# Kernel tuning notes

Measured on AMD Instinct MI355X. Metric: run time of the kernel, lower is better.

The kernel has to match this reference:

```python
import jax, jax.numpy as jnp
import numpy as np

# layer hyperparameters (init_kwargs)
SCORE_T = 0.05
IOU_T = 0.5
MAX_OUT = 300
BBOX_STD = np.array([0.1, 0.1, 0.2, 0.2], dtype=np.float32)


def setup_inputs() -> dict:
    key = jax.random.key(0)
    k1, k2, k3, k4 = jax.random.split(key, 4)
    B, N, C = 8, 2000, 81
    deltas = jax.random.normal(k1, (B, N, C, 4), jnp.float32) * 0.1
    class_logits = jax.random.normal(k2, (B, N, C), jnp.float32)
    # well-formed proposal boxes (y1,x1,y2,x2) in normalized coords + tag column
    cyx = jax.random.uniform(k3, (B, N, 2), jnp.float32, 0.1, 0.9)
    hw = jax.random.uniform(k4, (B, N, 2), jnp.float32, 0.05, 0.3)
    proposals = jnp.concatenate([cyx - hw * 0.5, cyx + hw * 0.5, jnp.ones((B, N, 1), jnp.float32)], axis=-1)
    return {"deltas": deltas, "class_logits": class_logits, "proposals": proposals}


def apply_regress(d, boxes):
    # d: [...,4] (dy,dx,dh,dw); boxes: [...,4] (y1,x1,y2,x2)
    h = boxes[..., 2] - boxes[..., 0]
    w = boxes[..., 3] - boxes[..., 1]
    cy = (boxes[..., 2] + boxes[..., 0]) * 0.5
    cx = (boxes[..., 3] + boxes[..., 1]) * 0.5
    d = d * jnp.asarray(BBOX_STD, d.dtype)
    cy = cy + d[..., 0] * h
    cx = cx + d[..., 1] * w
    h = h * jnp.exp(d[..., 2])
    w = w * jnp.exp(d[..., 3])
    return jnp.stack([cy - h * 0.5, cx - w * 0.5, cy + h * 0.5, cx + w * 0.5], axis=-1)


def box_iou(a, b):
    # a: [N,4], b: [M,4] -> [N,M]
    yx1 = jnp.maximum(a[:, None, :2], b[None, :, :2])
    yx2 = jnp.minimum(a[:, None, 2:], b[None, :, 2:])
    inter = jnp.prod(jnp.maximum(yx2 - yx1, 0.0), axis=-1)
    area_a = (a[:, 2] - a[:, 0]) * (a[:, 3] - a[:, 1])
    area_b = (b[:, 2] - b[:, 0]) * (b[:, 3] - b[:, 1])
    return inter / (area_a[:, None] + area_b[None, :] - inter + 1e-8)


def nms_one(boxes, scores, logits):
    # boxes [N,4], scores [N], logits [N,C]; greedy NMS, pad to MAX_OUT with tag column
    ious = box_iou(boxes, boxes)  # [N,N]
    live = jnp.where(scores > SCORE_T, scores, -1.0)

    def step(s, _):
        idx = jnp.argmax(s)
        ok = s[idx] > 0.0  # softmax scores are >0; -1.0 marks dead
        s = jnp.where(ious[idx] > IOU_T, -1.0, s)
        s = s.at[idx].set(-1.0)
        return s, (idx, ok)

    _, (idxs, oks) = jax.lax.scan(step, live, None, length=MAX_OUT)
    okf = oks.astype(boxes.dtype)[:, None]  # [MAX_OUT,1], 1=real box, 0=padding
    out_boxes = jnp.concatenate([boxes[idxs] * okf, okf], axis=-1)          # [MAX_OUT,5]
    out_scores = jnp.concatenate([scores[idxs][:, None] * okf, okf], axis=-1)  # [MAX_OUT,2]
    out_logits = logits[idxs] * okf                                          # [MAX_OUT,C]
    return out_boxes, out_scores, out_logits


def reference(deltas, class_logits, proposals):
    boxes_in = proposals[..., :-1]                         # drop tag -> [B,N,4]
    class_scores = jax.nn.softmax(class_logits, axis=-1)   # [B,N,C]
    fg_scores = jnp.max(class_scores[..., 1:], axis=-1)    # [B,N]
    fg_cls = jnp.argmax(class_scores[..., 1:], axis=-1) + 1  # [B,N] best fg class
    # select class-specific delta for the best foreground class
    sel_deltas = jnp.take_along_axis(deltas, fg_cls[..., None, None], axis=2)[..., 0, :]  # [B,N,4]
    detect_boxes = apply_regress(sel_deltas, boxes_in)      # [B,N,4]
    return jax.vmap(nms_one)(detect_boxes, fg_scores, class_logits)
```

## Files before the change

### kernel.cpp

```cpp
#include <hip/hip_runtime.h>

#define BATCH 8
#define NBOX 2000
#define NCLS 81
#define NPAD 2048
#define MAX_OUT 300
#define SCORE_T 0.05f
#define IOU_T 0.5f
#define MASK_WORDS 64

#define WS_BOXES   0
#define WS_SCORES  256000
#define WS_SKEY    320000
#define WS_SBOX    451072
#define WS_LARR    713216
#define WS_KLIST   713248
#define WS_KCOUNT  722848
#define WS_MASK    786432

__global__ void prep_kernel(const float* __restrict__ deltas,
                            const float* __restrict__ logits,
                            const float* __restrict__ proposals,
                            float4* __restrict__ boxes_out,
                            float* __restrict__ scores_out,
                            int* __restrict__ Larr) {
    int bn = blockIdx.x * blockDim.x + threadIdx.x;
    if (bn < BATCH) Larr[bn] = 0;
    if (bn >= BATCH * NBOX) return;

    const float* l = logits + (long)bn * NCLS;

    float M = l[0];
    #pragma unroll 4
    for (int c = 1; c < NCLS; ++c) M = fmaxf(M, l[c]);

    float S = 0.0f;
    float bl = -3.0e38f; int bc = 1;
    #pragma unroll 4
    for (int c = 0; c < NCLS; ++c) {
        float v = l[c];
        S += expf(v - M);
        if (c >= 1 && v > bl) { bl = v; bc = c; }
    }
    float score = expf(bl - M) / S;

    const float* p = proposals + (long)bn * 5;
    float y1 = p[0], x1 = p[1], y2 = p[2], x2 = p[3];
    float h = y2 - y1, w = x2 - x1;
    float cy = (y2 + y1) * 0.5f, cx = (x2 + x1) * 0.5f;

    const float* d = deltas + ((long)bn * NCLS + bc) * 4;
    float d0 = d[0] * 0.1f, d1 = d[1] * 0.1f, d2 = d[2] * 0.2f, d3 = d[3] * 0.2f;

    cy = cy + d0 * h;
    cx = cx + d1 * w;
    h = h * expf(d2);
    w = w * expf(d3);

    boxes_out[bn] = make_float4(cy - h * 0.5f, cx - w * 0.5f,
                                cy + h * 0.5f, cx + w * 0.5f);
    scores_out[bn] = score;
}

__global__ __launch_bounds__(512) void rank_kernel(
        const float* __restrict__ scores,
        const float4* __restrict__ boxes,
        unsigned long long* __restrict__ skey,
        float4* __restrict__ sbox,
        int* __restrict__ Larr) {
    int bid = blockIdx.x;
    int b = bid & 7, rb = bid >> 3;
    int t = threadIdx.x;

    __shared__ unsigned long long s_key[NPAD + 16];
    __shared__ int s_part[64][8];

    for (int c = t; c < NPAD; c += 512) {
        unsigned int bits = 0u;
        if (c < NBOX) bits = __float_as_uint(scores[b * NBOX + c]);
        s_key[c + (c >> 7)] =
            ((unsigned long long)bits << 32) |
            (unsigned long long)(0xFFFFFFFFu - (unsigned)c);
    }
    __syncthreads();

    int own = rb * 64 + (t >> 3);
    int seg = t & 7;
    unsigned long long mykey = s_key[own + (own >> 7)];
    int cnt = 0;
    int cbase = seg * 256;
    #pragma unroll 4
    for (int j = 0; j < 256; ++j) {
        int c = cbase + j;
        cnt += (s_key[c + (c >> 7)] > mykey) ? 1 : 0;
    }
    s_part[t >> 3][seg] = cnt;
    __syncthreads();

    if (t < 64) {
        int own2 = rb * 64 + t;
        unsigned long long key = s_key[own2 + (own2 >> 7)];
        int rank = s_part[t][0] + s_part[t][1] + s_part[t][2] + s_part[t][3]
                 + s_part[t][4] + s_part[t][5] + s_part[t][6] + s_part[t][7];
        skey[b * NPAD + rank] = key;
        unsigned int orig = 0xFFFFFFFFu - (unsigned int)key;
        float4 bx = make_float4(0.f, 0.f, 0.f, 0.f);
        if (orig < NBOX) bx = boxes[b * NBOX + orig];
        sbox[b * NPAD + rank] = bx;
        float sc = __uint_as_float((unsigned int)(key >> 32));
        if (sc > SCORE_T) atomicMax(&Larr[b], rank + 1);
    }
}

__global__ __launch_bounds__(512) void mask_kernel(
        const float4* __restrict__ sbox,
        const int* __restrict__ Larr,
        unsigned int* __restrict__ mask) {
    int bid = blockIdx.x;
    int b = bid & 7, rb = bid >> 3;
    int L = Larr[b];
    if (rb * 64 >= L) return;
    int t = threadIdx.x;

    __shared__ float4 s_bx[NPAD + 16];

    for (int c = t; c < NPAD; c += 512)
        s_bx[c + (c >> 7)] = sbox[b * NPAD + c];
    __syncthreads();

    int r   = rb * 64 + (t & 63);
    int seg = t >> 6;
    float4 rbx = s_bx[r + (r >> 7)];
    float rar = (rbx.z - rbx.x) * (rbx.w - rbx.y);
    unsigned int* outp = mask + (((size_t)(b * NPAD + r)) << 6);

    for (int w = 0; w < 8; ++w) {
        int wi = (seg << 3) + w;
        unsigned int bits = 0u;
        int colbase = wi << 5;
        if (colbase + 31 > r && colbase < L) {
            #pragma unroll 8
            for (int c2 = 0; c2 < 32; ++c2) {
                int col = colbase + c2;
                float4 ob = s_bx[col + (col >> 7)];
                float oa = (ob.z - ob.x) * (ob.w - ob.y);
                float yy1 = fmaxf(rbx.x, ob.x), xx1 = fmaxf(rbx.y, ob.y);
                float yy2 = fminf(rbx.z, ob.z), xx2 = fminf(rbx.w, ob.w);
                float inter = fmaxf(yy2 - yy1, 0.f) * fmaxf(xx2 - xx1, 0.f);
                float iou = inter / (rar + oa - inter + 1e-8f);
                bits |= (iou > IOU_T) ? (1u << c2) : 0u;
            }
        }
        outp[wi] = bits;
    }
}

__global__ __launch_bounds__(64) void walk_kernel(
        const int* __restrict__ Larr,
        const unsigned int* __restrict__ mask,
        int* __restrict__ klist,
        int* __restrict__ kcount) {
    int b = blockIdx.x;
    int lane = threadIdx.x;

    int L = Larr[b];
    int nset = L - (lane << 5);
    nset = nset < 0 ? 0 : (nset > 32 ? 32 : nset);
    unsigned int alive = (nset >= 32) ? 0xFFFFFFFFu
                        : ((nset <= 0) ? 0u : ((1u << nset) - 1u));

    const unsigned int* M = mask + ((size_t)b * NPAD) * MASK_WORDS;
    int* kl = klist + b * MAX_OUT;
    int kept = 0;

#define EXTRACT(cd)                                                          \
    {                                                                        \
        if (!aw && ne) {                                                     \
            int _w = (int)__builtin_ctzll(ne); ne &= ne - 1ull;              \
            wbase = _w << 5;                                                 \
            aw = (unsigned int)__builtin_amdgcn_readlane((int)alive, _w);    \
        }                                                                    \
        if (aw) { cd = wbase + (int)__builtin_ctz(aw); aw &= aw - 1u; }      \
    }
#define COMMIT(cd, rowd)                                                     \
    if (cd >= 0 && kept < MAX_OUT) {                                         \
        unsigned int _av =                                                   \
            (unsigned int)__builtin_amdgcn_readlane((int)alive, cd >> 5);    \
        if (_av & (1u << (cd & 31))) {                                       \
            if (lane == 0) kl[kept] = cd;                                    \
            kept++;                                                          \
            alive &= ~rowd;                                                  \
            if (lane == (cd >> 5)) alive &= ~(1u << (cd & 31));              \
        }                                                                    \
    }

    while (kept < MAX_OUT) {
        unsigned long long ne = __ballot(alive != 0u);
        if (!ne) break;
        unsigned int aw = 0u;
        int wbase = 0;
        int c0 = -1, c1 = -1, c2 = -1, c3 = -1, c4 = -1, c5 = -1,
            c6 = -1, c7 = -1, c8 = -1, c9 = -1, c10 = -1, c11 = -1;
        EXTRACT(c0); EXTRACT(c1); EXTRACT(c2); EXTRACT(c3);
        EXTRACT(c4); EXTRACT(c5); EXTRACT(c6); EXTRACT(c7);
        EXTRACT(c8); EXTRACT(c9); EXTRACT(c10); EXTRACT(c11);

        int s1 = (c1 >= 0) ? c1 : c0;
        int s2 = (c2 >= 0) ? c2 : c0;
        int s3 = (c3 >= 0) ? c3 : c0;
        int s4 = (c4 >= 0) ? c4 : c0;
        int s5 = (c5 >= 0) ? c5 : c0;
        int s6 = (c6 >= 0) ? c6 : c0;
        int s7 = (c7 >= 0) ? c7 : c0;
        int s8 = (c8 >= 0) ? c8 : c0;
        int s9 = (c9 >= 0) ? c9 : c0;
        int s10 = (c10 >= 0) ? c10 : c0;
        int s11 = (c11 >= 0) ? c11 : c0;

        unsigned int row0  = M[((size_t)c0  << 6) + lane];
        unsigned int row1  = M[((size_t)s1  << 6) + lane];
        unsigned int row2  = M[((size_t)s2  << 6) + lane];
        unsigned int row3  = M[((size_t)s3  << 6) + lane];
        unsigned int row4  = M[((size_t)s4  << 6) + lane];
        unsigned int row5  = M[((size_t)s5  << 6) + lane];
        unsigned int row6  = M[((size_t)s6  << 6) + lane];
        unsigned int row7  = M[((size_t)s7  << 6) + lane];
        unsigned int row8  = M[((size_t)s8  << 6) + lane];
        unsigned int row9  = M[((size_t)s9  << 6) + lane];
        unsigned int row10 = M[((size_t)s10 << 6) + lane];
        unsigned int row11 = M[((size_t)s11 << 6) + lane];

        if (lane == 0) kl[kept] = c0;
        kept++;
        alive &= ~row0;
        if (lane == (c0 >> 5)) alive &= ~(1u << (c0 & 31));

        COMMIT(c1, row1);  COMMIT(c2, row2);  COMMIT(c3, row3);
        COMMIT(c4, row4);  COMMIT(c5, row5);  COMMIT(c6, row6);
        COMMIT(c7, row7);  COMMIT(c8, row8);  COMMIT(c9, row9);
        COMMIT(c10, row10); COMMIT(c11, row11);
    }
#undef EXTRACT
#undef COMMIT

    if (lane == 0) kcount[b] = kept;
}

__global__ void out_kernel(const unsigned long long* __restrict__ skey,
                           const float4* __restrict__ sbox,
                           const int* __restrict__ klist,
                           const int* __restrict__ kcount,
                           const float* __restrict__ logits,
                           float* __restrict__ out) {
    int idx = blockIdx.x * blockDim.x + threadIdx.x;
    const int NB = BATCH * MAX_OUT * 5;
    const int NS = BATCH * MAX_OUT * 2;
    const int NL = BATCH * MAX_OUT * NCLS;
    if (idx >= NB + NS + NL) return;

    if (idx < NB) {
        int b = idx / (MAX_OUT * 5);
        int rem = idx - b * (MAX_OUT * 5);
        int k = rem / 5, c = rem - 5 * k;
        float v = 0.f;
        if (k < kcount[b]) {
            if (c == 4) v = 1.f;
            else {
                float4 bx = sbox[b * NPAD + klist[b * MAX_OUT + k]];
                v = (c == 0) ? bx.x : (c == 1) ? bx.y : (c == 2) ? bx.z : bx.w;
            }
        }
        out[idx] = v;
    } else if (idx < NB + NS) {
        int j = idx - NB;
        int b = j / (MAX_OUT * 2);
        int rem = j - b * (MAX_OUT * 2);
        int k = rem >> 1, c = rem & 1;
        float v = 0.f;
        if (k < kcount[b]) {
            if (c) v = 1.f;
            else {
                unsigned long long key = skey[b * NPAD + klist[b * MAX_OUT + k]];
                v = __uint_as_float((unsigned int)(key >> 32));
            }
        }
        out[idx] = v;
    } else {
        int j = idx - NB - NS;
        int b = j / (MAX_OUT * NCLS);
        int rem = j - b * (MAX_OUT * NCLS);
        int k = rem / NCLS, c = rem - NCLS * k;
        float v = 0.f;
        if (k < kcount[b]) {
            unsigned long long key = skey[b * NPAD + klist[b * MAX_OUT + k]];
            unsigned int orig = 0xFFFFFFFFu - (unsigned int)key;
            v = logits[((long)b * NBOX + orig) * NCLS + c];
        }
        out[idx] = v;
    }
}

extern "C" void kernel_launch(void* const* d_in, const int* in_sizes, int n_in,
                              void* d_out, int out_size, void* d_ws, size_t ws_size,
                              hipStream_t stream) {
    const float* deltas    = (const float*)d_in[0];
    const float* logits    = (const float*)d_in[1];
    const float* proposals = (const float*)d_in[2];
    float* out = (float*)d_out;

    char* ws = (char*)d_ws;
    float4* ws_boxes  = (float4*)(ws + WS_BOXES);
    float*  ws_scores = (float*)(ws + WS_SCORES);
    unsigned long long* ws_skey = (unsigned long long*)(ws + WS_SKEY);
    float4* ws_sbox   = (float4*)(ws + WS_SBOX);
    int*    ws_Larr   = (int*)(ws + WS_LARR);
    int*    ws_klist  = (int*)(ws + WS_KLIST);
    int*    ws_kcount = (int*)(ws + WS_KCOUNT);
    unsigned int* ws_mask = (unsigned int*)(ws + WS_MASK);

    prep_kernel<<<(BATCH * NBOX + 255) / 256, 256, 0, stream>>>(
        deltas, logits, proposals, ws_boxes, ws_scores, ws_Larr);
    rank_kernel<<<BATCH * (NPAD / 64), 512, 0, stream>>>(
        ws_scores, ws_boxes, ws_skey, ws_sbox, ws_Larr);
    mask_kernel<<<BATCH * (NPAD / 64), 512, 0, stream>>>(
        ws_sbox, ws_Larr, ws_mask);
    walk_kernel<<<BATCH, 64, 0, stream>>>(
        ws_Larr, ws_mask, ws_klist, ws_kcount);
    int total_out = BATCH * MAX_OUT * (5 + 2 + NCLS);
    out_kernel<<<(total_out + 255) / 256, 256, 0, stream>>>(
        ws_skey, ws_sbox, ws_klist, ws_kcount, logits, out);
}
```

Measured before the change: 117.1 us.

## Resolve NMS walk in 64-candidate windows using ballot-built suppression submatrix

Restructures the greedy NMS walk kernel. Each iteration gathers up to 64 alive candidates through a prefix scan into shared memory and loads their mask rows plus the transposed column bits. It builds a 64x64 suppression submatrix with ballots, so the greedy keep/suppress decisions inside the window resolve in registers. This replaces the old loop that speculated on 12 candidates per iteration, cutting the number of serial iterations and dependent global loads per kept box. The cost is 128 global loads per lane per iteration, heavy register use (arrays of 64), several syncthreads, and wasted work when few candidates survive.

```diff
diff --git a/kernel.cpp b/kernel.cpp
--- a/kernel.cpp
+++ b/kernel.cpp
@@ -8,6 +8,7 @@
 #define SCORE_T 0.05f
 #define IOU_T 0.5f
 #define MASK_WORDS 64
+#define WDEPTH 64
 
 #define WS_BOXES   0
 #define WS_SCORES  256000
@@ -163,6 +164,10 @@
     int b = blockIdx.x;
     int lane = threadIdx.x;
 
+    __shared__ int s_cand[WDEPTH];
+    __shared__ unsigned int s_clrw[64];
+    __shared__ int s_kl[MAX_OUT];
+
     int L = Larr[b];
     int nset = L - (lane << 5);
     nset = nset < 0 ? 0 : (nset > 32 ? 32 : nset);
@@ -170,80 +175,110 @@
                         : ((nset <= 0) ? 0u : ((1u << nset) - 1u));
 
     const unsigned int* M = mask + ((size_t)b * NPAD) * MASK_WORDS;
-    int* kl = klist + b * MAX_OUT;
     int kept = 0;
-
-#define EXTRACT(cd)                                                          \
-    {                                                                        \
-        if (!aw && ne) {                                                     \
-            int _w = (int)__builtin_ctzll(ne); ne &= ne - 1ull;              \
-            wbase = _w << 5;                                                 \
-            aw = (unsigned int)__builtin_amdgcn_readlane((int)alive, _w);    \
-        }                                                                    \
-        if (aw) { cd = wbase + (int)__builtin_ctz(aw); aw &= aw - 1u; }      \
-    }
-#define COMMIT(cd, rowd)                                                     \
-    if (cd >= 0 && kept < MAX_OUT) {                                         \
-        unsigned int _av =                                                   \
-            (unsigned int)__builtin_amdgcn_readlane((int)alive, cd >> 5);    \
-        if (_av & (1u << (cd & 31))) {                                       \
-            if (lane == 0) kl[kept] = cd;                                    \
-            kept++;                                                          \
-            alive &= ~rowd;                                                  \
-            if (lane == (cd >> 5)) alive &= ~(1u << (cd & 31));              \
-        }                                                                    \
-    }
 
     while (kept < MAX_OUT) {
         unsigned long long ne = __ballot(alive != 0u);
         if (!ne) break;
-        unsigned int aw = 0u;
-        int wbase = 0;
-        int c0 = -1, c1 = -1, c2 = -1, c3 = -1, c4 = -1, c5 = -1,
-            c6 = -1, c7 = -1, c8 = -1, c9 = -1, c10 = -1, c11 = -1;
-        EXTRACT(c0); EXTRACT(c1); EXTRACT(c2); EXTRACT(c3);
-        EXTRACT(c4); EXTRACT(c5); EXTRACT(c6); EXTRACT(c7);
-        EXTRACT(c8); EXTRACT(c9); EXTRACT(c10); EXTRACT(c11);
-
-        int s1 = (c1 >= 0) ? c1 : c0;
-        int s2 = (c2 >= 0) ? c2 : c0;
-        int s3 = (c3 >= 0) ? c3 : c0;
-        int s4 = (c4 >= 0) ? c4 : c0;
-        int s5 = (c5 >= 0) ? c5 : c0;
-        int s6 = (c6 >= 0) ? c6 : c0;
-        int s7 = (c7 >= 0) ? c7 : c0;
-        int s8 = (c8 >= 0) ? c8 : c0;
-        int s9 = (c9 >= 0) ? c9 : c0;
-        int s10 = (c10 >= 0) ? c10 : c0;
-        int s11 = (c11 >= 0) ? c11 : c0;
-
-        unsigned int row0  = M[((size_t)c0  << 6) + lane];
-        unsigned int row1  = M[((size_t)s1  << 6) + lane];
-        unsigned int row2  = M[((size_t)s2  << 6) + lane];
-        unsigned int row3  = M[((size_t)s3  << 6) + lane];
-        unsigned int row4  = M[((size_t)s4  << 6) + lane];
-        unsigned int row5  = M[((size_t)s5  << 6) + lane];
-        unsigned int row6  = M[((size_t)s6  << 6) + lane];
-        unsigned int row7  = M[((size_t)s7  << 6) + lane];
-        unsigned int row8  = M[((size_t)s8  << 6) + lane];
-        unsigned int row9  = M[((size_t)s9  << 6) + lane];
-        unsigned int row10 = M[((size_t)s10 << 6) + lane];
-        unsigned int row11 = M[((size_t)s11 << 6) + lane];
-
-        if (lane == 0) kl[kept] = c0;
-        kept++;
-        alive &= ~row0;
-        if (lane == (c0 >> 5)) alive &= ~(1u << (c0 & 31));
-
-        COMMIT(c1, row1);  COMMIT(c2, row2);  COMMIT(c3, row3);
-        COMMIT(c4, row4);  COMMIT(c5, row5);  COMMIT(c6, row6);
-        COMMIT(c7, row7);  COMMIT(c8, row8);  COMMIT(c9, row9);
-        COMMIT(c10, row10); COMMIT(c11, row11);
-    }
-#undef EXTRACT
-#undef COMMIT
+
+        int mypc = __builtin_popcount(alive);
+        int incl = mypc;
+        #pragma unroll
+        for (int off = 1; off < 64; off <<= 1) {
+            int n = __shfl_up(incl, off);
+            if (lane >= off) incl += n;
+        }
+        int excl = incl - mypc;
+        int total = __builtin_amdgcn_readlane(incl, 63);
+        int ncand = total < WDEPTH ? total : WDEPTH;
+
+        {
+            unsigned int aw = alive;
+            int pos = excl;
+            while (aw && pos < WDEPTH) {
+                int bit = (int)__builtin_ctz(aw);
+                aw &= aw - 1u;
+                s_cand[pos] = (lane << 5) + bit;
+                pos++;
+            }
+        }
+        __syncthreads();
+
+        int candv = s_cand[lane < ncand ? lane : 0];
+
+        int cdsc[WDEPTH];
+        #pragma unroll
+        for (int d = 0; d < WDEPTH; ++d)
+            cdsc[d] = __builtin_amdgcn_readlane(candv, d);
+
+        unsigned int rowA[WDEPTH];
+        #pragma unroll
+        for (int d = 0; d < WDEPTH; ++d)
+            rowA[d] = M[((size_t)cdsc[d] << 6) + lane];
+
+        unsigned int colw[WDEPTH];
+        int myw = candv >> 5;
+        #pragma unroll
+        for (int e = 0; e < WDEPTH; ++e)
+            colw[e] = M[((size_t)cdsc[e] << 6) + myw];
+
+        int sh = candv & 31;
+        unsigned int colv_lo = 0u, colv_hi = 0u;
+        #pragma unroll
+        for (int e = 0; e < 32; ++e)
+            colv_lo |= ((colw[e] >> sh) & 1u) << e;
+        #pragma unroll
+        for (int e = 32; e < WDEPTH; ++e)
+            colv_hi |= ((colw[e] >> sh) & 1u) << (e - 32);
+
+        unsigned long long sub[WDEPTH];
+        #pragma unroll
+        for (int e = 0; e < 32; ++e)
+            sub[e] = __ballot(((colv_lo >> e) & 1u) != 0u);
+        #pragma unroll
+        for (int e = 32; e < WDEPTH; ++e)
+            sub[e] = __ballot(((colv_hi >> (e - 32)) & 1u) != 0u);
+
+        unsigned long long live =
+            (ncand >= 64) ? ~0ull : ((1ull << ncand) - 1ull);
+        unsigned long long committed = 0ull;
+        int kept_base = kept;
+        #pragma unroll
+        for (int e = 0; e < WDEPTH; ++e) {
+            if (kept < MAX_OUT && ((live >> e) & 1ull)) {
+                committed |= 1ull << e;
+                kept++;
+                live &= ~sub[e];
+            }
+        }
+
+        unsigned int acc = 0u;
+        #pragma unroll
+        for (int d = 0; d < WDEPTH; ++d) {
+            unsigned int m = 0u - (unsigned int)((committed >> d) & 1ull);
+            acc |= rowA[d] & m;
+        }
+        alive &= ~acc;
+
+        s_clrw[lane] = 0u;
+        __syncthreads();
+        if (lane < ncand && ((committed >> lane) & 1ull))
+            atomicOr(&s_clrw[candv >> 5], 1u << (candv & 31));
+        __syncthreads();
+        alive &= ~s_clrw[lane];
+
+        if (lane < ncand && ((committed >> lane) & 1ull)) {
+            int pos = kept_base +
+                (int)__builtin_popcountll(committed & ((1ull << lane) - 1ull));
+            s_kl[pos] = candv;
+        }
+        __syncthreads();
+    }
 
     if (lane == 0) kcount[b] = kept;
+    __syncthreads();
+    for (int k = lane; k < kept; k += 64)
+        klist[b * MAX_OUT + k] = s_kl[k];
 }
 
 __global__ void out_kernel(const unsigned long long* __restrict__ skey,
```

New measurement: 108.2 us. -7.5%, faster.
